# Kernel tuning notes

Measured on AMD Instinct MI355X. Metric: run time of the kernel, lower is better.

## Reference

```python
import jax, jax.numpy as jnp
import numpy as np


def setup_inputs() -> dict:
    key = jax.random.key(0)
    x = jax.random.normal(key, (256, 64, 4096), dtype=jnp.float32)
    return {"x": x}


def _mat_shrinkage(cov, n):
    # cov: [B, p, p]; Rao-Blackwell Ledoit-Wolf shrinkage toward scaled identity
    p = cov.shape[-1]
    I = jnp.eye(p, dtype=cov.dtype)[None]                      # [1, p, p]
    trace = jnp.trace(cov, axis1=-2, axis2=-1)[:, None, None]  # [B, 1, 1]
    F_hat = trace / p * I                                      # [B, p, p]
    # tr(C @ C) without materializing C@C
    second_trace = jnp.einsum('bij,bji->b', cov, cov)[:, None, None]
    numerator = (n - 2) / n * second_trace + trace ** 2
    denominator = (n + 2) * (second_trace - trace ** 2 / p)
    rho = jnp.minimum(numerator / denominator, 1.0)
    return rho * F_hat + (1.0 - rho) * cov


def reference(x):
    # x: [B, C, M]
    B, C, M = x.shape
    x_mu = jnp.mean(x, axis=2, keepdims=True)          # [B, C, 1]
    x_cnt = x - x_mu                                    # [B, C, M]
    cov = jnp.einsum('bcm,bdm->bcd', x_cnt, x_cnt) / M  # [B, C, C]
    cov = _mat_shrinkage(cov, n=M)
    L = jnp.linalg.cholesky(jnp.linalg.inv(cov))        # [B, C, C], lower
    # Z = L^T @ x_cnt
    Z = jnp.einsum('bdc,bdm->bcm', L, x_cnt)            # [B, C, M]
    return Z
```

## Files before the change

### kernel.cpp

```cpp
#include <hip/hip_runtime.h>

#define B_ 256
#define C_ 64
#define M_ 4096
#define SLICES 8
#define MSLICE (M_ / SLICES)

__global__ __launch_bounds__(64) void k_gram(const float* __restrict__ x,
                                             float* __restrict__ Gp,
                                             float* __restrict__ Mp) {
    const int b = blockIdx.x;
    const int s = blockIdx.y;
    const int t = threadIdx.x;
    const int tc = t >> 3, td = t & 7;

    __shared__ float Xt[32][68];
    __shared__ float ms[64][9];

    float acc[8][8];
#pragma unroll
    for (int i = 0; i < 8; ++i)
#pragma unroll
        for (int j = 0; j < 8; ++j) acc[i][j] = 0.f;
    float msum[8] = {0, 0, 0, 0, 0, 0, 0, 0};

    const float* xb = x + (size_t)b * C_ * M_ + s * MSLICE;

    for (int stage = 0; stage < MSLICE / 32; ++stage) {
        const float* xs = xb + stage * 32;
        __syncthreads();
#pragma unroll
        for (int k = 0; k < 8; ++k) {
            int f4 = t + 64 * k;
            int c = f4 >> 3;
            int m4 = f4 & 7;
            float4 v = *(const float4*)(xs + (size_t)c * M_ + m4 * 4);
            msum[k] += v.x + v.y + v.z + v.w;
            Xt[m4 * 4 + 0][c] = v.x;
            Xt[m4 * 4 + 1][c] = v.y;
            Xt[m4 * 4 + 2][c] = v.z;
            Xt[m4 * 4 + 3][c] = v.w;
        }
        __syncthreads();
#pragma unroll 4
        for (int m = 0; m < 32; ++m) {
            float a[8], bb[8];
            *(float4*)&a[0]  = *(const float4*)&Xt[m][tc * 8];
            *(float4*)&a[4]  = *(const float4*)&Xt[m][tc * 8 + 4];
            *(float4*)&bb[0] = *(const float4*)&Xt[m][td * 8];
            *(float4*)&bb[4] = *(const float4*)&Xt[m][td * 8 + 4];
#pragma unroll
            for (int i = 0; i < 8; ++i)
#pragma unroll
                for (int j = 0; j < 8; ++j)
                    acc[i][j] = fmaf(a[i], bb[j], acc[i][j]);
        }
    }

    float* gp = Gp + ((size_t)(b * SLICES + s)) * 4096;
#pragma unroll
    for (int i = 0; i < 8; ++i) {
        *(float4*)&gp[(tc * 8 + i) * 64 + td * 8 + 0] =
            make_float4(acc[i][0], acc[i][1], acc[i][2], acc[i][3]);
        *(float4*)&gp[(tc * 8 + i) * 64 + td * 8 + 4] =
            make_float4(acc[i][4], acc[i][5], acc[i][6], acc[i][7]);
    }
#pragma unroll
    for (int k = 0; k < 8; ++k) ms[tc + 8 * k][td] = msum[k];
    __syncthreads();
    {
        float ssum = 0.f;
#pragma unroll
        for (int l = 0; l < 8; ++l) ssum += ms[t][l];
        Mp[(size_t)(b * SLICES + s) * 64 + t] = ssum;
    }
}

__global__ __launch_bounds__(256) void k_solve(const float* __restrict__ Gp,
                                               const float* __restrict__ Mp,
                                               float* __restrict__ Lg,
                                               float* __restrict__ wmug) {
    const int b = blockIdx.x;
    const int t = threadIdx.x;
    __shared__ float C[64][65];
    __shared__ float X[64][65];
    __shared__ float A[64][65];
    __shared__ float mu[64];
    __shared__ float red[256];
    __shared__ float sc[4];

    for (int idx = t; idx < 4096; idx += 256) {
        float ssum = 0.f;
        for (int sl = 0; sl < SLICES; ++sl)
            ssum += Gp[((size_t)(b * SLICES + sl)) * 4096 + idx];
        C[idx >> 6][idx & 63] = ssum;
    }
    if (t < 64) {
        float ssum = 0.f;
        for (int sl = 0; sl < SLICES; ++sl)
            ssum += Mp[(size_t)(b * SLICES + sl) * 64 + t];
        mu[t] = ssum * (1.0f / M_);
    }
    __syncthreads();
    for (int idx = t; idx < 4096; idx += 256) {
        int i = idx >> 6, j = idx & 63;
        C[i][j] = C[i][j] * (1.0f / M_) - mu[i] * mu[j];
    }
    __syncthreads();
    float trp = 0.f, stp = 0.f;
    for (int idx = t; idx < 4096; idx += 256) {
        int i = idx >> 6, j = idx & 63;
        float v = C[i][j];
        stp += v * C[j][i];
        if (i == j) trp += v;
    }
    red[t] = stp;
    __syncthreads();
    for (int off = 128; off > 0; off >>= 1) {
        if (t < off) red[t] += red[t + off];
        __syncthreads();
    }
    if (t == 0) sc[1] = red[0];
    __syncthreads();
    red[t] = trp;
    __syncthreads();
    for (int off = 128; off > 0; off >>= 1) {
        if (t < off) red[t] += red[t + off];
        __syncthreads();
    }
    if (t == 0) {
        float tr = red[0], st = sc[1];
        const float n = (float)M_, p = 64.f;
        float num = (n - 2.f) / n * st + tr * tr;
        float den = (n + 2.f) * (st - tr * tr / p);
        float rho = fminf(num / den, 1.0f);
        sc[0] = tr;
        sc[2] = rho;
    }
    __syncthreads();
    {
        float rho = sc[2], tr = sc[0];
        float diagadd = rho * tr / 64.f;
        for (int idx = t; idx < 4096; idx += 256) {
            int i = idx >> 6, j = idx & 63;
            float v = (1.f - rho) * C[i][j];
            if (i == j) v += diagadd;
            C[i][j] = v;
        }
    }
    __syncthreads();
    for (int k = 0; k < 64; ++k) {
        if (t == 0) C[k][k] = sqrtf(C[k][k]);
        __syncthreads();
        float dinv = 1.0f / C[k][k];
        for (int i = k + 1 + t; i < 64; i += 256) C[i][k] *= dinv;
        __syncthreads();
        for (int idx = t; idx < 4096; idx += 256) {
            int i = idx >> 6, j = idx & 63;
            if (j > k && i >= j) C[i][j] -= C[i][k] * C[j][k];
        }
        __syncthreads();
    }
    if (t < 64) {
        const int c = t;
        for (int i = 0; i < 64; ++i) {
            float ssum = (i == c) ? 1.0f : 0.0f;
            for (int j = 0; j < i; ++j) ssum -= C[i][j] * X[c][j];
            X[c][i] = ssum / C[i][i];
        }
    }
    __syncthreads();
    for (int idx = t; idx < 4096; idx += 256) {
        int i = idx >> 6, j = idx & 63;
        float ssum = 0.f;
#pragma unroll 8
        for (int k = 0; k < 64; ++k) ssum += X[i][k] * X[j][k];
        A[i][j] = ssum;
    }
    __syncthreads();
    for (int k = 0; k < 64; ++k) {
        if (t == 0) A[k][k] = sqrtf(A[k][k]);
        __syncthreads();
        float dinv = 1.0f / A[k][k];
        for (int i = k + 1 + t; i < 64; i += 256) A[i][k] *= dinv;
        __syncthreads();
        for (int idx = t; idx < 4096; idx += 256) {
            int i = idx >> 6, j = idx & 63;
            if (j > k && i >= j) A[i][j] -= A[i][k] * A[j][k];
        }
        __syncthreads();
    }
    for (int idx = t; idx < 4096; idx += 256) {
        int d = idx >> 6, c = idx & 63;
        Lg[(size_t)b * 4096 + idx] = (c <= d) ? A[d][c] : 0.f;
    }
    if (t < 64) {
        float ssum = 0.f;
        for (int d = t; d < 64; ++d) ssum += A[d][t] * mu[d];
        wmug[b * 64 + t] = ssum;
    }
}

__global__ __launch_bounds__(128) void k_apply(const float* __restrict__ x,
                                               const float* __restrict__ Lg,
                                               const float* __restrict__ wmug,
                                               float* __restrict__ out) {
    const int b = blockIdx.x;
    const int s = blockIdx.y;
    const int t = threadIdx.x;
    const int tc = t >> 4, tm = t & 15;

    __shared__ float Lt[64][68];
    __shared__ float Xm[64][68];
    __shared__ float wsh[64];

#pragma unroll
    for (int k = 0; k < 8; ++k) {
        int f4 = t + 128 * k;
        int d = f4 >> 4, c4 = f4 & 15;
        float4 v = *(const float4*)(Lg + (size_t)b * 4096 + d * 64 + c4 * 4);
        *(float4*)&Lt[d][c4 * 4] = v;
    }
    if (t < 64) wsh[t] = wmug[b * 64 + t];

    const float* xb = x + (size_t)b * C_ * M_;
    float* ob = out + (size_t)b * C_ * M_;

    for (int sub = 0; sub < 8; ++sub) {
        const int m0 = s * MSLICE + sub * 64;
        __syncthreads();
#pragma unroll
        for (int k = 0; k < 8; ++k) {
            int f4 = t + 128 * k;
            int d = f4 >> 4, m4 = f4 & 15;
            float4 v = *(const float4*)(xb + (size_t)d * M_ + m0 + m4 * 4);
            *(float4*)&Xm[d][m4 * 4] = v;
        }
        __syncthreads();
        float acc[8][4];
#pragma unroll
        for (int i = 0; i < 8; ++i)
            acc[i][0] = acc[i][1] = acc[i][2] = acc[i][3] = 0.f;
#pragma unroll 4
        for (int d = 0; d < 64; ++d) {
            float a[8];
            *(float4*)&a[0] = *(const float4*)&Lt[d][tc * 8];
            *(float4*)&a[4] = *(const float4*)&Lt[d][tc * 8 + 4];
            float4 bv = *(const float4*)&Xm[d][tm * 4];
#pragma unroll
            for (int i = 0; i < 8; ++i) {
                acc[i][0] = fmaf(a[i], bv.x, acc[i][0]);
                acc[i][1] = fmaf(a[i], bv.y, acc[i][1]);
                acc[i][2] = fmaf(a[i], bv.z, acc[i][2]);
                acc[i][3] = fmaf(a[i], bv.w, acc[i][3]);
            }
        }
#pragma unroll
        for (int i = 0; i < 8; ++i) {
            int c = tc * 8 + i;
            float w = wsh[c];
            float4 o = make_float4(acc[i][0] - w, acc[i][1] - w,
                                   acc[i][2] - w, acc[i][3] - w);
            *(float4*)(ob + (size_t)c * M_ + m0 + tm * 4) = o;
        }
    }
}

extern "C" void kernel_launch(void* const* d_in, const int* in_sizes, int n_in,
                              void* d_out, int out_size, void* d_ws, size_t ws_size,
                              hipStream_t stream) {
    const float* x = (const float*)d_in[0];
    float* out = (float*)d_out;

    const size_t gp_elems = (size_t)B_ * SLICES * 4096;
    const size_t mp_elems = (size_t)B_ * SLICES * 64;
    const size_t lg_elems = (size_t)B_ * 4096;
    const size_t wm_elems = (size_t)B_ * 64;

    float *Gp, *Mp, *Lg, *Wm;
    const size_t need_all = (gp_elems + mp_elems + lg_elems + wm_elems) * 4;
    if (ws_size >= need_all) {
        float* w = (float*)d_ws;
        Gp = w;
        Mp = Gp + gp_elems;
        Lg = Mp + mp_elems;
        Wm = Lg + lg_elems;
    } else {
        Gp = out;
        Mp = Gp + gp_elems;
        float* w = (float*)d_ws;
        Lg = w;
        Wm = Lg + lg_elems;
    }

    k_gram<<<dim3(B_, SLICES), 64, 0, stream>>>(x, Gp, Mp);
    k_solve<<<dim3(B_), 256, 0, stream>>>(Gp, Mp, Lg, Wm);
    k_apply<<<dim3(B_, SLICES), 128, 0, stream>>>(x, Lg, Wm, out);
}
```

Before: 804.3 us.

## Fuse gram, solve and apply into one per-batch kernel with UL Cholesky

Replaces the three-kernel pipeline with a single kernel per batch element. It computes the Gram matrix with four waves that each own an M quarter, reduces them in shared memory, then does shrinkage and an upper-lower (reverse) Cholesky. That factor is inverted by triangular solve to get L directly, replacing the inverse plus second Cholesky. Register-prefetched loads overlap global reads with compute. This removes the workspace round trips and two launches, and roughly halves the solve work. The cost is only 256 blocks, so one per batch, which limits parallelism and latency hiding on a large GPU.

```diff
diff --git a/kernel.cpp b/kernel.cpp
--- a/kernel.cpp
+++ b/kernel.cpp
@@ -3,52 +3,71 @@
 #define B_ 256
 #define C_ 64
 #define M_ 4096
-#define SLICES 8
-#define MSLICE (M_ / SLICES)
-
-__global__ __launch_bounds__(64) void k_gram(const float* __restrict__ x,
-                                             float* __restrict__ Gp,
-                                             float* __restrict__ Mp) {
+
+__global__ __launch_bounds__(256) void k_fused(const float* __restrict__ x,
+                                               float* __restrict__ out) {
     const int b = blockIdx.x;
-    const int s = blockIdx.y;
     const int t = threadIdx.x;
-    const int tc = t >> 3, td = t & 7;
-
-    __shared__ float Xt[32][68];
-    __shared__ float ms[64][9];
+    const int w = t >> 6;
+    const int l = t & 63;
+
+    __shared__ float St[64][68];
+    __shared__ float Cw[64][68];
+    __shared__ float Ww[64][68];
+    __shared__ float ms[64][17];
+    __shared__ float mu[64];
+    __shared__ float red[256];
+    __shared__ float ucol[64];
+    __shared__ float wmu[64];
+    __shared__ float sc[4];
+
+    const float* xb = x + (size_t)b * (C_ * M_);
+    float* ob = out + (size_t)b * (C_ * M_);
+
+    const int tc = l >> 3, td = l & 7;
+    const int cl = l >> 2;
+    const int m4 = l & 3;
 
     float acc[8][8];
 #pragma unroll
     for (int i = 0; i < 8; ++i)
 #pragma unroll
         for (int j = 0; j < 8; ++j) acc[i][j] = 0.f;
-    float msum[8] = {0, 0, 0, 0, 0, 0, 0, 0};
-
-    const float* xb = x + (size_t)b * C_ * M_ + s * MSLICE;
-
-    for (int stage = 0; stage < MSLICE / 32; ++stage) {
-        const float* xs = xb + stage * 32;
-        __syncthreads();
-#pragma unroll
-        for (int k = 0; k < 8; ++k) {
-            int f4 = t + 64 * k;
-            int c = f4 >> 3;
-            int m4 = f4 & 7;
-            float4 v = *(const float4*)(xs + (size_t)c * M_ + m4 * 4);
+    float msum[4] = {0.f, 0.f, 0.f, 0.f};
+
+    const int mbase = w * 1024;
+    float4 r[4];
+#pragma unroll
+    for (int k = 0; k < 4; ++k)
+        r[k] = *(const float4*)(xb + (size_t)(cl + 16 * k) * M_ + mbase + m4 * 4);
+
+    for (int s = 0; s < 64; ++s) {
+        __syncthreads();
+#pragma unroll
+        for (int k = 0; k < 4; ++k) {
+            float4 v = r[k];
             msum[k] += v.x + v.y + v.z + v.w;
-            Xt[m4 * 4 + 0][c] = v.x;
-            Xt[m4 * 4 + 1][c] = v.y;
-            Xt[m4 * 4 + 2][c] = v.z;
-            Xt[m4 * 4 + 3][c] = v.w;
-        }
-        __syncthreads();
-#pragma unroll 4
-        for (int m = 0; m < 32; ++m) {
+            const int row = w * 16 + m4 * 4;
+            const int c = cl + 16 * k;
+            St[row + 0][c] = v.x;
+            St[row + 1][c] = v.y;
+            St[row + 2][c] = v.z;
+            St[row + 3][c] = v.w;
+        }
+        if (s < 63) {
+#pragma unroll
+            for (int k = 0; k < 4; ++k)
+                r[k] = *(const float4*)(xb + (size_t)(cl + 16 * k) * M_ +
+                                        mbase + (s + 1) * 16 + m4 * 4);
+        }
+        __syncthreads();
+#pragma unroll 2
+        for (int m = 0; m < 16; ++m) {
             float a[8], bb[8];
-            *(float4*)&a[0]  = *(const float4*)&Xt[m][tc * 8];
-            *(float4*)&a[4]  = *(const float4*)&Xt[m][tc * 8 + 4];
-            *(float4*)&bb[0] = *(const float4*)&Xt[m][td * 8];
-            *(float4*)&bb[4] = *(const float4*)&Xt[m][td * 8 + 4];
+            *(float4*)&a[0]  = *(const float4*)&St[w * 16 + m][tc * 8];
+            *(float4*)&a[4]  = *(const float4*)&St[w * 16 + m][tc * 8 + 4];
+            *(float4*)&bb[0] = *(const float4*)&St[w * 16 + m][td * 8];
+            *(float4*)&bb[4] = *(const float4*)&St[w * 16 + m][td * 8 + 4];
 #pragma unroll
             for (int i = 0; i < 8; ++i)
 #pragma unroll
@@ -56,212 +75,192 @@
                     acc[i][j] = fmaf(a[i], bb[j], acc[i][j]);
         }
     }
-
-    float* gp = Gp + ((size_t)(b * SLICES + s)) * 4096;
-#pragma unroll
-    for (int i = 0; i < 8; ++i) {
-        *(float4*)&gp[(tc * 8 + i) * 64 + td * 8 + 0] =
-            make_float4(acc[i][0], acc[i][1], acc[i][2], acc[i][3]);
-        *(float4*)&gp[(tc * 8 + i) * 64 + td * 8 + 4] =
-            make_float4(acc[i][4], acc[i][5], acc[i][6], acc[i][7]);
-    }
-#pragma unroll
-    for (int k = 0; k < 8; ++k) ms[tc + 8 * k][td] = msum[k];
-    __syncthreads();
-    {
-        float ssum = 0.f;
-#pragma unroll
-        for (int l = 0; l < 8; ++l) ssum += ms[t][l];
-        Mp[(size_t)(b * SLICES + s) * 64 + t] = ssum;
-    }
-}
-
-__global__ __launch_bounds__(256) void k_solve(const float* __restrict__ Gp,
-                                               const float* __restrict__ Mp,
-                                               float* __restrict__ Lg,
-                                               float* __restrict__ wmug) {
-    const int b = blockIdx.x;
-    const int t = threadIdx.x;
-    __shared__ float C[64][65];
-    __shared__ float X[64][65];
-    __shared__ float A[64][65];
-    __shared__ float mu[64];
-    __shared__ float red[256];
-    __shared__ float sc[4];
-
-    for (int idx = t; idx < 4096; idx += 256) {
-        float ssum = 0.f;
-        for (int sl = 0; sl < SLICES; ++sl)
-            ssum += Gp[((size_t)(b * SLICES + sl)) * 4096 + idx];
-        C[idx >> 6][idx & 63] = ssum;
-    }
-    if (t < 64) {
-        float ssum = 0.f;
-        for (int sl = 0; sl < SLICES; ++sl)
-            ssum += Mp[(size_t)(b * SLICES + sl) * 64 + t];
-        mu[t] = ssum * (1.0f / M_);
+#pragma unroll
+    for (int k = 0; k < 4; ++k) ms[cl + 16 * k][w * 4 + m4] = msum[k];
+    __syncthreads();
+
+    if (w == 1) {
+#pragma unroll
+        for (int i = 0; i < 8; ++i) {
+            *(float4*)&Ww[tc * 8 + i][td * 8]     = make_float4(acc[i][0], acc[i][1], acc[i][2], acc[i][3]);
+            *(float4*)&Ww[tc * 8 + i][td * 8 + 4] = make_float4(acc[i][4], acc[i][5], acc[i][6], acc[i][7]);
+        }
+        float s = 0.f;
+#pragma unroll
+        for (int q = 0; q < 16; ++q) s += ms[l][q];
+        mu[l] = s * (1.0f / M_);
+    } else if (w == 2) {
+#pragma unroll
+        for (int i = 0; i < 8; ++i) {
+            *(float4*)&Cw[tc * 8 + i][td * 8]     = make_float4(acc[i][0], acc[i][1], acc[i][2], acc[i][3]);
+            *(float4*)&Cw[tc * 8 + i][td * 8 + 4] = make_float4(acc[i][4], acc[i][5], acc[i][6], acc[i][7]);
+        }
+    } else if (w == 3) {
+#pragma unroll
+        for (int i = 0; i < 8; ++i) {
+            *(float4*)&St[tc * 8 + i][td * 8]     = make_float4(acc[i][0], acc[i][1], acc[i][2], acc[i][3]);
+            *(float4*)&St[tc * 8 + i][td * 8 + 4] = make_float4(acc[i][4], acc[i][5], acc[i][6], acc[i][7]);
+        }
+    }
+    __syncthreads();
+    if (w == 0) {
+#pragma unroll
+        for (int i = 0; i < 8; ++i) {
+            float4 p0 = *(const float4*)&Ww[tc * 8 + i][td * 8];
+            float4 p1 = *(const float4*)&Cw[tc * 8 + i][td * 8];
+            float4 p2 = *(const float4*)&St[tc * 8 + i][td * 8];
+            float4 q0 = *(const float4*)&Ww[tc * 8 + i][td * 8 + 4];
+            float4 q1 = *(const float4*)&Cw[tc * 8 + i][td * 8 + 4];
+            float4 q2 = *(const float4*)&St[tc * 8 + i][td * 8 + 4];
+            float4 lo = make_float4(acc[i][0] + p0.x + p1.x + p2.x,
+                                    acc[i][1] + p0.y + p1.y + p2.y,
+                                    acc[i][2] + p0.z + p1.z + p2.z,
+                                    acc[i][3] + p0.w + p1.w + p2.w);
+            float4 hi = make_float4(acc[i][4] + q0.x + q1.x + q2.x,
+                                    acc[i][5] + q0.y + q1.y + q2.y,
+                                    acc[i][6] + q0.z + q1.z + q2.z,
+                                    acc[i][7] + q0.w + q1.w + q2.w);
+            *(float4*)&Cw[tc * 8 + i][td * 8]     = lo;
+            *(float4*)&Cw[tc * 8 + i][td * 8 + 4] = hi;
+        }
     }
     __syncthreads();
     for (int idx = t; idx < 4096; idx += 256) {
         int i = idx >> 6, j = idx & 63;
-        C[i][j] = C[i][j] * (1.0f / M_) - mu[i] * mu[j];
-    }
-    __syncthreads();
-    float trp = 0.f, stp = 0.f;
-    for (int idx = t; idx < 4096; idx += 256) {
-        int i = idx >> 6, j = idx & 63;
-        float v = C[i][j];
-        stp += v * C[j][i];
-        if (i == j) trp += v;
-    }
-    red[t] = stp;
-    __syncthreads();
-    for (int off = 128; off > 0; off >>= 1) {
-        if (t < off) red[t] += red[t + off];
-        __syncthreads();
-    }
-    if (t == 0) sc[1] = red[0];
-    __syncthreads();
-    red[t] = trp;
-    __syncthreads();
-    for (int off = 128; off > 0; off >>= 1) {
-        if (t < off) red[t] += red[t + off];
-        __syncthreads();
-    }
-    if (t == 0) {
-        float tr = red[0], st = sc[1];
-        const float n = (float)M_, p = 64.f;
-        float num = (n - 2.f) / n * st + tr * tr;
-        float den = (n + 2.f) * (st - tr * tr / p);
-        float rho = fminf(num / den, 1.0f);
-        sc[0] = tr;
-        sc[2] = rho;
-    }
-    __syncthreads();
+        Cw[i][j] = Cw[i][j] * (1.0f / M_) - mu[i] * mu[j];
+    }
+    __syncthreads();
+
     {
-        float rho = sc[2], tr = sc[0];
-        float diagadd = rho * tr / 64.f;
+        float trp = 0.f, stp = 0.f;
         for (int idx = t; idx < 4096; idx += 256) {
             int i = idx >> 6, j = idx & 63;
-            float v = (1.f - rho) * C[i][j];
-            if (i == j) v += diagadd;
-            C[i][j] = v;
-        }
-    }
-    __syncthreads();
-    for (int k = 0; k < 64; ++k) {
-        if (t == 0) C[k][k] = sqrtf(C[k][k]);
-        __syncthreads();
-        float dinv = 1.0f / C[k][k];
-        for (int i = k + 1 + t; i < 64; i += 256) C[i][k] *= dinv;
-        __syncthreads();
+            float v = Cw[i][j];
+            stp = fmaf(v, Cw[j][i], stp);
+            if (i == j) trp += v;
+        }
+        red[t] = stp;
+        __syncthreads();
+        for (int off = 128; off > 0; off >>= 1) {
+            if (t < off) red[t] += red[t + off];
+            __syncthreads();
+        }
+        if (t == 0) sc[1] = red[0];
+        __syncthreads();
+        red[t] = trp;
+        __syncthreads();
+        for (int off = 128; off > 0; off >>= 1) {
+            if (t < off) red[t] += red[t + off];
+            __syncthreads();
+        }
+        if (t == 0) {
+            float tr = red[0], st = sc[1];
+            const float n = (float)M_, p = 64.f;
+            float num = (n - 2.f) / n * st + tr * tr;
+            float den = (n + 2.f) * (st - tr * tr / p);
+            float rho = fminf(num / den, 1.0f);
+            sc[0] = tr;
+            sc[2] = rho;
+        }
+        __syncthreads();
+        float rho = sc[2], tr = sc[0];
+        float dadd = rho * tr * (1.0f / 64.0f);
         for (int idx = t; idx < 4096; idx += 256) {
             int i = idx >> 6, j = idx & 63;
-            if (j > k && i >= j) C[i][j] -= C[i][k] * C[j][k];
-        }
-        __syncthreads();
-    }
+            float v = (1.f - rho) * Cw[i][j];
+            if (i == j) v += dadd;
+            Cw[i][j] = v;
+        }
+    }
+
+    for (int k = 63; k >= 0; --k) {
+        __syncthreads();
+        float dkk = sqrtf(Cw[k][k]);
+        float dinv = 1.0f / dkk;
+        for (int i = t; i < k; i += 256) ucol[i] = Cw[i][k] * dinv;
+        if (t == 0) ucol[k] = dkk;
+        __syncthreads();
+        const int nel = (k * (k + 1)) >> 1;
+        for (int e = t; e < nel; e += 256) {
+            int j = (int)((sqrtf((float)(8 * e + 1)) - 1.0f) * 0.5f);
+            if (e < ((j * (j + 1)) >> 1)) --j;
+            else if (e >= (((j + 1) * (j + 2)) >> 1)) ++j;
+            int i = e - ((j * (j + 1)) >> 1);
+            Cw[i][j] = fmaf(-ucol[i], ucol[j], Cw[i][j]);
+        }
+        for (int i = t; i <= k; i += 256) Cw[i][k] = ucol[i];
+    }
+    __syncthreads();
+
     if (t < 64) {
-        const int c = t;
-        for (int i = 0; i < 64; ++i) {
-            float ssum = (i == c) ? 1.0f : 0.0f;
-            for (int j = 0; j < i; ++j) ssum -= C[i][j] * X[c][j];
-            X[c][i] = ssum / C[i][i];
-        }
-    }
-    __syncthreads();
-    for (int idx = t; idx < 4096; idx += 256) {
-        int i = idx >> 6, j = idx & 63;
-        float ssum = 0.f;
-#pragma unroll 8
-        for (int k = 0; k < 64; ++k) ssum += X[i][k] * X[j][k];
-        A[i][j] = ssum;
-    }
-    __syncthreads();
-    for (int k = 0; k < 64; ++k) {
-        if (t == 0) A[k][k] = sqrtf(A[k][k]);
-        __syncthreads();
-        float dinv = 1.0f / A[k][k];
-        for (int i = k + 1 + t; i < 64; i += 256) A[i][k] *= dinv;
-        __syncthreads();
-        for (int idx = t; idx < 4096; idx += 256) {
-            int i = idx >> 6, j = idx & 63;
-            if (j > k && i >= j) A[i][j] -= A[i][k] * A[j][k];
-        }
-        __syncthreads();
+        const int j = t;
+        Ww[j][j] = 1.0f / Cw[j][j];
+        for (int i = j - 1; i >= 0; --i) {
+            float s0 = 0.f, s1 = 0.f;
+            int lq = i + 1;
+            for (; lq + 1 <= j; lq += 2) {
+                s0 = fmaf(Cw[i][lq], Ww[lq][j], s0);
+                s1 = fmaf(Cw[i][lq + 1], Ww[lq + 1][j], s1);
+            }
+            if (lq <= j) s0 = fmaf(Cw[i][lq], Ww[lq][j], s0);
+            Ww[i][j] = -(s0 + s1) / Cw[i][i];
+        }
+    }
+    __syncthreads();
+    if (t < 64) {
+        float s = 0.f;
+        for (int d = t; d < 64; ++d) s = fmaf(Ww[t][d], mu[d], s);
+        wmu[t] = s;
     }
     for (int idx = t; idx < 4096; idx += 256) {
         int d = idx >> 6, c = idx & 63;
-        Lg[(size_t)b * 4096 + idx] = (c <= d) ? A[d][c] : 0.f;
-    }
-    if (t < 64) {
-        float ssum = 0.f;
-        for (int d = t; d < 64; ++d) ssum += A[d][t] * mu[d];
-        wmug[b * 64 + t] = ssum;
-    }
-}
-
-__global__ __launch_bounds__(128) void k_apply(const float* __restrict__ x,
-                                               const float* __restrict__ Lg,
-                                               const float* __restrict__ wmug,
-                                               float* __restrict__ out) {
-    const int b = blockIdx.x;
-    const int s = blockIdx.y;
-    const int t = threadIdx.x;
-    const int tc = t >> 4, tm = t & 15;
-
-    __shared__ float Lt[64][68];
-    __shared__ float Xm[64][68];
-    __shared__ float wsh[64];
-
-#pragma unroll
-    for (int k = 0; k < 8; ++k) {
-        int f4 = t + 128 * k;
-        int d = f4 >> 4, c4 = f4 & 15;
-        float4 v = *(const float4*)(Lg + (size_t)b * 4096 + d * 64 + c4 * 4);
-        *(float4*)&Lt[d][c4 * 4] = v;
-    }
-    if (t < 64) wsh[t] = wmug[b * 64 + t];
-
-    const float* xb = x + (size_t)b * C_ * M_;
-    float* ob = out + (size_t)b * C_ * M_;
-
-    for (int sub = 0; sub < 8; ++sub) {
-        const int m0 = s * MSLICE + sub * 64;
-        __syncthreads();
-#pragma unroll
-        for (int k = 0; k < 8; ++k) {
-            int f4 = t + 128 * k;
-            int d = f4 >> 4, m4 = f4 & 15;
-            float4 v = *(const float4*)(xb + (size_t)d * M_ + m0 + m4 * 4);
-            *(float4*)&Xm[d][m4 * 4] = v;
-        }
-        __syncthreads();
-        float acc[8][4];
-#pragma unroll
-        for (int i = 0; i < 8; ++i)
-            acc[i][0] = acc[i][1] = acc[i][2] = acc[i][3] = 0.f;
-#pragma unroll 4
-        for (int d = 0; d < 64; ++d) {
+        Cw[d][c] = (d >= c) ? Ww[c][d] : 0.f;
+    }
+
+    const int tc5 = t >> 5;
+    const int tm5 = t & 31;
+    const int cld = t >> 4;
+    const int m45 = t & 15;
+    const int d0 = w * 16;
+
+    float4 r2[4];
+#pragma unroll
+    for (int k = 0; k < 4; ++k)
+        r2[k] = *(const float4*)(xb + (size_t)(cld + 16 * k) * M_ + m45 * 4);
+
+    for (int ch = 0; ch < 64; ++ch) {
+        const int m0 = ch * 64;
+        __syncthreads();
+#pragma unroll
+        for (int k = 0; k < 4; ++k)
+            *(float4*)&St[cld + 16 * k][m45 * 4] = r2[k];
+        if (ch < 63) {
+#pragma unroll
+            for (int k = 0; k < 4; ++k)
+                r2[k] = *(const float4*)(xb + (size_t)(cld + 16 * k) * M_ +
+                                         m0 + 64 + m45 * 4);
+        }
+        __syncthreads();
+        float a2[8][2];
+#pragma unroll
+        for (int i = 0; i < 8; ++i) a2[i][0] = a2[i][1] = 0.f;
+        for (int d = d0; d < 64; ++d) {
             float a[8];
-            *(float4*)&a[0] = *(const float4*)&Lt[d][tc * 8];
-            *(float4*)&a[4] = *(const float4*)&Lt[d][tc * 8 + 4];
-            float4 bv = *(const float4*)&Xm[d][tm * 4];
+            *(float4*)&a[0] = *(const float4*)&Cw[d][tc5 * 8];
+            *(float4*)&a[4] = *(const float4*)&Cw[d][tc5 * 8 + 4];
+            float2 bv = *(const float2*)&St[d][tm5 * 2];
 #pragma unroll
             for (int i = 0; i < 8; ++i) {
-                acc[i][0] = fmaf(a[i], bv.x, acc[i][0]);
-                acc[i][1] = fmaf(a[i], bv.y, acc[i][1]);
-                acc[i][2] = fmaf(a[i], bv.z, acc[i][2]);
-                acc[i][3] = fmaf(a[i], bv.w, acc[i][3]);
+                a2[i][0] = fmaf(a[i], bv.x, a2[i][0]);
+                a2[i][1] = fmaf(a[i], bv.y, a2[i][1]);
             }
         }
 #pragma unroll
         for (int i = 0; i < 8; ++i) {
-            int c = tc * 8 + i;
-            float w = wsh[c];
-            float4 o = make_float4(acc[i][0] - w, acc[i][1] - w,
-                                   acc[i][2] - w, acc[i][3] - w);
-            *(float4*)(ob + (size_t)c * M_ + m0 + tm * 4) = o;
+            const int c = tc5 * 8 + i;
+            float wv = wmu[c];
+            float2 o = make_float2(a2[i][0] - wv, a2[i][1] - wv);
+            *(float2*)(ob + (size_t)c * M_ + m0 + tm5 * 2) = o;
         }
     }
 }
@@ -271,29 +270,5 @@
                               hipStream_t stream) {
     const float* x = (const float*)d_in[0];
     float* out = (float*)d_out;
-
-    const size_t gp_elems = (size_t)B_ * SLICES * 4096;
-    const size_t mp_elems = (size_t)B_ * SLICES * 64;
-    const size_t lg_elems = (size_t)B_ * 4096;
-    const size_t wm_elems = (size_t)B_ * 64;
-
-    float *Gp, *Mp, *Lg, *Wm;
-    const size_t need_all = (gp_elems + mp_elems + lg_elems + wm_elems) * 4;
-    if (ws_size >= need_all) {
-        float* w = (float*)d_ws;
-        Gp = w;
-        Mp = Gp + gp_elems;
-        Lg = Mp + mp_elems;
-        Wm = Lg + lg_elems;
-    } else {
-        Gp = out;
-        Mp = Gp + gp_elems;
-        float* w = (float*)d_ws;
-        Lg = w;
-        Wm = Lg + lg_elems;
-    }
-
-    k_gram<<<dim3(B_, SLICES), 64, 0, stream>>>(x, Gp, Mp);
-    k_solve<<<dim3(B_), 256, 0, stream>>>(Gp, Mp, Lg, Wm);
-    k_apply<<<dim3(B_, SLICES), 128, 0, stream>>>(x, Lg, Wm, out);
+    k_fused<<<dim3(B_), 256, 0, stream>>>(x, out);
 }
```

Measured after the change: 789.5 us. Within noise of the previous version (-1.8%).
